# Performance work log

Hardware: AMD Instinct MI355X
Metric: run time of the kernel (lower is better)

## Reference

```python
import jax, jax.numpy as jnp
import numpy as np


def setup_inputs() -> dict:
    key = jax.random.key(0)
    k1, k2, k3, k4 = jax.random.split(key, 4)
    B, S, DIN, DOUT = 4, 4096, 512, 128
    x = jax.random.normal(k1, (B, S, DIN), dtype=jnp.float32)
    Wq = jax.random.normal(k2, (DIN, DOUT), dtype=jnp.float32) * 0.02
    Wk = jax.random.normal(k3, (DIN, DOUT), dtype=jnp.float32) * 0.02
    Wv = jax.random.normal(k4, (DIN, DOUT), dtype=jnp.float32) * 0.02
    return {"x": x, "Wq": Wq, "Wk": Wk, "Wv": Wv}


def reference(x, Wq, Wk, Wv):
    # x: [B, S, d_in]; projections (bias-free Linear)
    q = jnp.einsum('bsd,de->bse', x, Wq)  # [B, S, d_out]
    k = jnp.einsum('bsd,de->bse', x, Wk)
    v = jnp.einsum('bsd,de->bse', x, Wv)
    d_out = k.shape[-1]
    scores = jnp.einsum('bqe,bke->bqk', q, k) / jnp.sqrt(jnp.float32(d_out))  # [B, S, S]
    S = x.shape[1]
    causal = jnp.tril(jnp.ones((S, S), dtype=bool))  # True where attending allowed
    scores = jnp.where(causal[None], scores, jnp.float32(-jnp.inf))
    attn = jax.nn.softmax(scores, axis=-1)
    # dropout p=0.0 -> identity (eval mode)
    return jnp.einsum('bqk,bke->bqe', attn, v)  # [B, S, d_out]
```

## Files before the change

kernel.cpp:

```cpp
#include <hip/hip_runtime.h>

typedef __bf16 bf16x8 __attribute__((ext_vector_type(8)));
typedef float f32x4 __attribute__((ext_vector_type(4)));
typedef unsigned short u16;
typedef unsigned int u32;
typedef u16 u16x8 __attribute__((ext_vector_type(8)));
typedef u16 u16x4 __attribute__((ext_vector_type(4)));
typedef u32 u32x4 __attribute__((ext_vector_type(4)));

__device__ __forceinline__ u16 f2bf(float f) {
    u32 u = __builtin_bit_cast(u32, f);
    u += 0x7fffu + ((u >> 16) & 1u);
    return (u16)(u >> 16);
}
__device__ __forceinline__ float bf2f(u16 v) {
    return __builtin_bit_cast(float, (u32)v << 16);
}
__device__ __forceinline__ u32 cvtpk(float a, float b) {
    u32 d;
    asm("v_cvt_pk_bf16_f32 %0, %1, %2" : "=v"(d) : "v"(a), "v"(b));
    return d;
}
__device__ __forceinline__ f32x4 mfma16(u16x8 a, u16x8 b, f32x4 c) {
    return __builtin_amdgcn_mfma_f32_16x16x32_bf16(
        __builtin_bit_cast(bf16x8, a), __builtin_bit_cast(bf16x8, b), c, 0, 0, 0);
}

#define GLOAD16(SRC, DST)                                                     \
    __builtin_amdgcn_global_load_lds(                                         \
        (const __attribute__((address_space(1))) unsigned int*)(SRC),         \
        (__attribute__((address_space(3))) unsigned int*)(DST), 16, 0, 0)

__device__ __forceinline__ int ldsAddr(int r, int c) {
    return r * 128 + (((c >> 3) ^ (r & 7)) << 3) + (c & 7);
}

__global__ __launch_bounds__(256) void prep_w(
    const float* __restrict__ Wq, const float* __restrict__ Wk,
    const float* __restrict__ Wv, u16* __restrict__ wf)
{
    int flat = blockIdx.x * 256 + threadIdx.x;
    int widx = flat >> 13, rem = flat & 8191;
    int n = rem >> 10, ds = (rem >> 6) & 15, lane = rem & 63;
    int l16 = lane & 15, g = lane >> 4;
    const float* W = (widx == 0) ? Wq : (widx == 1 ? Wk : Wv);
    const float sc = (widx == 0) ? (0.08838834764831845f * 1.4426950408889634f) : 1.0f;
    u16x8 v;
    #pragma unroll
    for (int j = 0; j < 8; ++j)
        v[j] = f2bf(W[(size_t)(ds * 32 + 8 * g + j) * 128 + n * 16 + l16] * sc);
    *(u16x8*)&wf[(size_t)flat * 8] = v;
}

__global__ __launch_bounds__(256) void prep_x(
    const float* __restrict__ x, u16* __restrict__ xf)
{
    __shared__ u16 T[16 * 512];
    const int rb = blockIdx.x, t = threadIdx.x;
    const int row = t >> 4, colb = (t & 15) * 32;
    const float* src = x + (size_t)(rb * 16 + row) * 512 + colb;
    #pragma unroll
    for (int i = 0; i < 4; ++i) {
        float4 va = *(const float4*)(src + i * 8);
        float4 vb = *(const float4*)(src + i * 8 + 4);
        u16x8 v;
        v[0] = f2bf(va.x); v[1] = f2bf(va.y); v[2] = f2bf(va.z); v[3] = f2bf(va.w);
        v[4] = f2bf(vb.x); v[5] = f2bf(vb.y); v[6] = f2bf(vb.z); v[7] = f2bf(vb.w);
        int chunk = ((colb >> 3) + i) ^ (row & 7);
        *(u16x8*)&T[row * 512 + chunk * 8] = v;
    }
    __syncthreads();
    #pragma unroll
    for (int ii = 0; ii < 4; ++ii) {
        int flatF = ii * 256 + t;
        int ds = flatF >> 6, lane = flatF & 63;
        int l16 = lane & 15, g = lane >> 4;
        int chunk = (4 * ds + g) ^ (l16 & 7);
        u16x8 v = *(const u16x8*)&T[l16 * 512 + chunk * 8];
        *(u16x8*)&xf[(((size_t)rb * 16 + ds) * 64 + lane) * 8] = v;
    }
}

__global__ __launch_bounds__(256) void qkv2(
    const u16* __restrict__ xf, const u16* __restrict__ wf,
    u16* __restrict__ Qf, u16* __restrict__ Kf, u16* __restrict__ Vf)
{
    __shared__ u16 T4[4][16 * 128];
    const int tid = threadIdx.x, lane = tid & 63, wid = tid >> 6;
    const int g = lane >> 4, l16 = lane & 15;
    const int widx = blockIdx.y;
    const int rb0 = (blockIdx.x * 128 + wid * 32) >> 4;
    const u16* WfB = wf + (size_t)widx * 8192 * 8;
    u16* T = T4[wid];

    const f32x4 fz = {0.f, 0.f, 0.f, 0.f};
    f32x4 acc0[8], acc1[8];
    #pragma unroll
    for (int n = 0; n < 8; ++n) { acc0[n] = fz; acc1[n] = fz; }

    #pragma unroll 4
    for (int ds = 0; ds < 16; ++ds) {
        u16x8 a0 = *(const u16x8*)&xf[(((size_t)rb0 * 16 + ds) * 64 + lane) * 8];
        u16x8 a1 = *(const u16x8*)&xf[(((size_t)(rb0 + 1) * 16 + ds) * 64 + lane) * 8];
        #pragma unroll
        for (int n = 0; n < 8; ++n) {
            u16x8 b = *(const u16x8*)&WfB[((size_t)(n * 16 + ds) * 64 + lane) * 8];
            acc0[n] = mfma16(a0, b, acc0[n]);
            acc1[n] = mfma16(a1, b, acc1[n]);
        }
    }

    #pragma unroll
    for (int h = 0; h < 2; ++h) {
        const int rbg = rb0 + h;
        #pragma unroll
        for (int n = 0; n < 8; ++n) {
            f32x4 a = h ? acc1[n] : acc0[n];
            #pragma unroll
            for (int r = 0; r < 4; ++r)
                T[ldsAddr(4 * g + r, n * 16 + l16)] = f2bf(a[r]);
        }
        if (widx < 2) {
            u16* dst = (widx == 0) ? Qf : Kf;
            #pragma unroll
            for (int ds = 0; ds < 4; ++ds) {
                int chunk = (4 * ds + g) ^ (l16 & 7);
                u16x8 v = *(const u16x8*)&T[l16 * 128 + chunk * 8];
                *(u16x8*)&dst[(((size_t)rbg * 4 + ds) * 64 + lane) * 8] = v;
            }
        } else {
            const int kb = rbg >> 2, ksel = (rbg >> 1) & 1, g0 = (rbg & 1) * 2;
            #pragma unroll
            for (int s = 0; s < 4; ++s) {
                int flat = s * 64 + lane;
                int e = flat >> 5, gg = (flat >> 4) & 1, l16p = flat & 15;
                u16x8 v;
                #pragma unroll
                for (int j = 0; j < 8; ++j)
                    v[j] = T[ldsAddr(8 * gg + j, e * 16 + l16p)];
                *(u16x8*)&Vf[((((size_t)kb * 2 + ksel) * 8 + e) * 64
                              + (g0 + gg) * 16 + l16p) * 8] = v;
            }
        }
    }
}

__global__ __launch_bounds__(256, 2) void attn6(
    const u16* __restrict__ Qf, const u16* __restrict__ Kf,
    const u16* __restrict__ Vf, float* __restrict__ out,
    u16* __restrict__ po, float2* __restrict__ pml, int split)
{
    __shared__ u16 lds[2][16384];
    const int tid = threadIdx.x, lane = tid & 63, wid = tid >> 6;
    const int g = lane >> 4, l16 = lane & 15;

    int b, qb, c, u;
    if (split) {
        const int xcd = blockIdx.x & 7;
        b = xcd >> 1;
        int jb = 271 - ((xcd & 1) * 136 + (blockIdx.x >> 3));
        u = 0;
        while ((u + 1) * (u + 2) <= jb) ++u;
        int r = jb - u * (u + 1);
        int hi = (r >= u + 1) ? 1 : 0;
        qb = 2 * u + hi;
        c = r - hi * (u + 1);
    } else {
        b = blockIdx.x & 3;
        qb = blockIdx.x >> 2;
        c = 0; u = 0;
    }
    const int q0 = qb * 128 + wid * 32;
    const int k_lo = c * 256;
    const int k_hi = min(k_lo + (split ? 256 : 4096), qb * 128 + 128);
    const int nch = u + 1;
    const int wklen = q0 + 32;

    {
        const u16* src;
        if (wid < 2) src = Kf + (size_t)(b * 256 + (k_lo >> 4)) * 2048 + wid * 4096;
        else         src = Vf + (size_t)(b * 64 + (k_lo >> 6)) * 8192 + (wid - 2) * 4096;
        u16* dst = &lds[0][wid * 4096];
        #pragma unroll
        for (int j = 0; j < 8; ++j)
            GLOAD16(src + j * 512 + lane * 8, dst + j * 512);
    }
    const int rbq = b * 256 + qb * 8 + wid * 2;
    u16x8 qf0[4], qf1[4];
    #pragma unroll
    for (int ds = 0; ds < 4; ++ds) {
        qf0[ds] = *(const u16x8*)&Qf[(((size_t)rbq * 4 + ds) * 64 + lane) * 8];
        qf1[ds] = *(const u16x8*)&Qf[(((size_t)(rbq + 1) * 4 + ds) * 64 + lane) * 8];
    }

    const f32x4 fz = {0.f, 0.f, 0.f, 0.f};
    f32x4 o0[8], o1[8];
    #pragma unroll
    for (int e = 0; e < 8; ++e) { o0[e] = fz; o1[e] = fz; }
    float m0 = -3e38f, m1 = -3e38f, l0 = 0.f, l1 = 0.f;

    const int srcA = l16 + ((g & 1) << 5);
    const int srcB = srcA + 16;
    const bool hiSel = (g >= 2);

    __syncthreads();

    int bufsel = 0;
    for (int k0 = k_lo; k0 < k_hi; k0 += 64) {
        if (k0 + 64 < k_hi) {
            const u16* src;
            if (wid < 2) src = Kf + (size_t)(b * 256 + ((k0 + 64) >> 4)) * 2048 + wid * 4096;
            else         src = Vf + (size_t)(b * 64 + ((k0 + 64) >> 6)) * 8192 + (wid - 2) * 4096;
            u16* dst = &lds[bufsel ^ 1][wid * 4096];
            #pragma unroll
            for (int j = 0; j < 8; ++j)
                GLOAD16(src + j * 512 + lane * 8, dst + j * 512);
        }
        if (k0 < wklen) {
            const u16* Kl = &lds[bufsel][0];
            const u16* Vl = &lds[bufsel][8192];
            f32x4 st0[4], st1[4];
            #pragma unroll
            for (int kt = 0; kt < 4; ++kt) {
                st0[kt] = fz; st1[kt] = fz;
                #pragma unroll
                for (int ds = 0; ds < 4; ++ds) {
                    u16x8 kf = *(const u16x8*)&Kl[(kt * 4 + ds) * 512 + lane * 8];
                    st0[kt] = mfma16(kf, qf0[ds], st0[kt]);
                    st1[kt] = mfma16(kf, qf1[ds], st1[kt]);
                }
            }
            if (k0 + 63 > q0) {
                int qg = q0 + l16;
                #pragma unroll
                for (int kt = 0; kt < 4; ++kt)
                    #pragma unroll
                    for (int r = 0; r < 4; ++r)
                        if (k0 + kt * 16 + g * 4 + r > qg) st0[kt][r] = -1e30f;
            }
            if (k0 + 63 > q0 + 16) {
                int qg = q0 + 16 + l16;
                #pragma unroll
                for (int kt = 0; kt < 4; ++kt)
                    #pragma unroll
                    for (int r = 0; r < 4; ++r)
                        if (k0 + kt * 16 + g * 4 + r > qg) st1[kt][r] = -1e30f;
            }
            u32 pk0[4][2], pk1[4][2];
            {
                float pm = -3e38f;
                #pragma unroll
                for (int kt = 0; kt < 4; ++kt)
                    pm = fmaxf(pm, fmaxf(fmaxf(st0[kt][0], st0[kt][1]), fmaxf(st0[kt][2], st0[kt][3])));
                pm = fmaxf(pm, __shfl_xor(pm, 16));
                pm = fmaxf(pm, __shfl_xor(pm, 32));
                if (!__all(pm - m0 <= 10.0f)) {
                    float mnew = fmaxf(m0, pm);
                    float alpha = exp2f(m0 - mnew);
                    l0 *= alpha;
                    #pragma unroll
                    for (int e = 0; e < 8; ++e)
                        #pragma unroll
                        for (int r = 0; r < 4; ++r) o0[e][r] *= alpha;
                    m0 = mnew;
                }
                float lsum = 0.f;
                #pragma unroll
                for (int kt = 0; kt < 4; ++kt) {
                    float p0 = exp2f(st0[kt][0] - m0), p1 = exp2f(st0[kt][1] - m0);
                    float p2 = exp2f(st0[kt][2] - m0), p3 = exp2f(st0[kt][3] - m0);
                    lsum += (p0 + p1) + (p2 + p3);
                    pk0[kt][0] = cvtpk(p0, p1);
                    pk0[kt][1] = cvtpk(p2, p3);
                }
                lsum += __shfl_xor(lsum, 16);
                lsum += __shfl_xor(lsum, 32);
                l0 += lsum;
            }
            {
                float pm = -3e38f;
                #pragma unroll
                for (int kt = 0; kt < 4; ++kt)
                    pm = fmaxf(pm, fmaxf(fmaxf(st1[kt][0], st1[kt][1]), fmaxf(st1[kt][2], st1[kt][3])));
                pm = fmaxf(pm, __shfl_xor(pm, 16));
                pm = fmaxf(pm, __shfl_xor(pm, 32));
                if (!__all(pm - m1 <= 10.0f)) {
                    float mnew = fmaxf(m1, pm);
                    float alpha = exp2f(m1 - mnew);
                    l1 *= alpha;
                    #pragma unroll
                    for (int e = 0; e < 8; ++e)
                        #pragma unroll
                        for (int r = 0; r < 4; ++r) o1[e][r] *= alpha;
                    m1 = mnew;
                }
                float lsum = 0.f;
                #pragma unroll
                for (int kt = 0; kt < 4; ++kt) {
                    float p0 = exp2f(st1[kt][0] - m1), p1 = exp2f(st1[kt][1] - m1);
                    float p2 = exp2f(st1[kt][2] - m1), p3 = exp2f(st1[kt][3] - m1);
                    lsum += (p0 + p1) + (p2 + p3);
                    pk1[kt][0] = cvtpk(p0, p1);
                    pk1[kt][1] = cvtpk(p2, p3);
                }
                lsum += __shfl_xor(lsum, 16);
                lsum += __shfl_xor(lsum, 32);
                l1 += lsum;
            }
            #pragma unroll
            for (int ksel = 0; ksel < 2; ++ksel) {
                u32 a0 = __shfl((int)pk0[2 * ksel][0], srcA), b0 = __shfl((int)pk0[2 * ksel + 1][0], srcA);
                u32 a1 = __shfl((int)pk0[2 * ksel][1], srcA), b1 = __shfl((int)pk0[2 * ksel + 1][1], srcA);
                u32 a2 = __shfl((int)pk0[2 * ksel][0], srcB), b2 = __shfl((int)pk0[2 * ksel + 1][0], srcB);
                u32 a3 = __shfl((int)pk0[2 * ksel][1], srcB), b3 = __shfl((int)pk0[2 * ksel + 1][1], srcB);
                u32x4 d0 = { hiSel ? b0 : a0, hiSel ? b1 : a1, hiSel ? b2 : a2, hiSel ? b3 : a3 };
                u16x8 pf0 = __builtin_bit_cast(u16x8, d0);
                u32 c0 = __shfl((int)pk1[2 * ksel][0], srcA), e0 = __shfl((int)pk1[2 * ksel + 1][0], srcA);
                u32 c1 = __shfl((int)pk1[2 * ksel][1], srcA), e1 = __shfl((int)pk1[2 * ksel + 1][1], srcA);
                u32 c2 = __shfl((int)pk1[2 * ksel][0], srcB), e2 = __shfl((int)pk1[2 * ksel + 1][0], srcB);
                u32 c3 = __shfl((int)pk1[2 * ksel][1], srcB), e3 = __shfl((int)pk1[2 * ksel + 1][1], srcB);
                u32x4 d1 = { hiSel ? e0 : c0, hiSel ? e1 : c1, hiSel ? e2 : c2, hiSel ? e3 : c3 };
                u16x8 pf1 = __builtin_bit_cast(u16x8, d1);
                #pragma unroll
                for (int e = 0; e < 8; ++e) {
                    u16x8 vf = *(const u16x8*)&Vl[(ksel * 8 + e) * 512 + lane * 8];
                    o0[e] = mfma16(vf, pf0, o0[e]);
                    o1[e] = mfma16(vf, pf1, o1[e]);
                }
            }
        }
        __syncthreads();
        bufsel ^= 1;
    }

    if (nch == 1) {
        float inv0 = 1.0f / l0, inv1 = 1.0f / l1;
        float* op0 = out + ((size_t)b * 4096 + q0 + l16) * 128;
        float* op1 = out + ((size_t)b * 4096 + q0 + 16 + l16) * 128;
        #pragma unroll
        for (int e = 0; e < 8; ++e) {
            f32x4 v0 = o0[e], v1 = o1[e];
            #pragma unroll
            for (int r = 0; r < 4; ++r) { v0[r] *= inv0; v1[r] *= inv1; }
            *(f32x4*)&op0[e * 16 + g * 4] = v0;
            *(f32x4*)&op1[e * 16 + g * 4] = v1;
        }
    } else {
        const int slot = b * 272 + u * (u + 1) + (qb & 1) * (u + 1) + c;
        u16* pp0 = po + ((size_t)slot * 128 + wid * 32 + l16) * 128;
        u16* pp1 = pp0 + 16 * 128;
        #pragma unroll
        for (int e = 0; e < 8; ++e) {
            u16x4 v0, v1;
            #pragma unroll
            for (int r = 0; r < 4; ++r) { v0[r] = f2bf(o0[e][r]); v1[r] = f2bf(o1[e][r]); }
            *(u16x4*)&pp0[e * 16 + g * 4] = v0;
            *(u16x4*)&pp1[e * 16 + g * 4] = v1;
        }
        if (g == 0) {
            pml[(size_t)slot * 128 + wid * 32 + l16] = make_float2(m0, l0);
            pml[(size_t)slot * 128 + wid * 32 + 16 + l16] = make_float2(m1, l1);
        }
    }
}

__global__ __launch_bounds__(256) void merge6(
    const u16* __restrict__ po, const float2* __restrict__ pml,
    float* __restrict__ out)
{
    int gid = blockIdx.x * 256 + threadIdx.x;
    int colg = gid & 31;
    int rowid = gid >> 5;
    int b = rowid / 3840;
    int rr = rowid - b * 3840;
    int qb = (rr >> 7) + 2;
    int qr = rr & 127;
    int u = qb >> 1;
    int nch = u + 1;
    int slot0 = b * 272 + u * (u + 1) + (qb & 1) * (u + 1);

    float ms = -3e38f;
    #pragma unroll 1
    for (int cc = 0; cc < nch; ++cc)
        ms = fmaxf(ms, pml[(size_t)(slot0 + cc) * 128 + qr].x);
    float den = 0.f;
    f32x4 num = {0.f, 0.f, 0.f, 0.f};
    #pragma unroll 1
    for (int cc = 0; cc < nch; ++cc) {
        float2 ml = pml[(size_t)(slot0 + cc) * 128 + qr];
        float w = exp2f(ml.x - ms);
        den += w * ml.y;
        u16x4 pv = *(const u16x4*)&po[((size_t)(slot0 + cc) * 128 + qr) * 128 + colg * 4];
        #pragma unroll
        for (int j = 0; j < 4; ++j) num[j] += w * bf2f(pv[j]);
    }
    float inv = 1.0f / den;
    f32x4 res = { num[0] * inv, num[1] * inv, num[2] * inv, num[3] * inv };
    *(f32x4*)&out[((size_t)b * 4096 + qb * 128 + qr) * 128 + colg * 4] = res;
}

extern "C" void kernel_launch(void* const* d_in, const int* in_sizes, int n_in,
                              void* d_out, int out_size, void* d_ws, size_t ws_size,
                              hipStream_t stream) {
    (void)in_sizes; (void)n_in; (void)out_size;
    const float* x  = (const float*)d_in[0];
    const float* Wq = (const float*)d_in[1];
    const float* Wk = (const float*)d_in[2];
    const float* Wv = (const float*)d_in[3];
    float* out = (float*)d_out;

    u16* Qf = (u16*)d_ws;
    u16* Kf = Qf + 2097152;
    u16* Vf = Kf + 2097152;
    u16* xf = Vf + 2097152;
    u16* wf = xf + 8388608;
    u16* po = xf;
    float2* pml = (float2*)(po + (size_t)1088 * 128 * 128);

    const size_t fixed_b = (size_t)3 * 2097152 * 2;
    const size_t part_b  = (size_t)1088 * 128 * (128 * 2 + 8);
    const int split = (ws_size >= fixed_b + part_b) ? 1 : 0;

    prep_w<<<96, 256, 0, stream>>>(Wq, Wk, Wv, wf);
    prep_x<<<1024, 256, 0, stream>>>(x, xf);
    qkv2<<<dim3(128, 3), 256, 0, stream>>>(xf, wf, Qf, Kf, Vf);
    attn6<<<split ? 1088 : 128, 256, 0, stream>>>(Qf, Kf, Vf, out, po, pml, split);
    if (split) merge6<<<1920, 256, 0, stream>>>(po, pml, out);
}
```

Baseline: 89.96 us.

## Double attention query tile to 256 rows with 8-wave blocks

The attention kernel now uses 512-thread blocks of 8 waves covering 256 query rows, so each K/V tile staged in LDS serves twice as many queries. The split-K work decomposition is re-indexed to a triangular layout over 256-row query blocks (544 blocks instead of 1088), and the merge kernel and partial buffers are resized to match. The aim is to cut K/V global-to-LDS traffic per query and the number of partial results to merge. In exchange there are fewer blocks to fill the GPU, and the wider causal diagonal tile wastes more masked work per block.

```diff
diff --git a/kernel.cpp b/kernel.cpp
--- a/kernel.cpp
+++ b/kernel.cpp
@@ -145,7 +145,7 @@
     }
 }
 
-__global__ __launch_bounds__(256, 2) void attn6(
+__global__ __launch_bounds__(512, 4) void attn8(
     const u16* __restrict__ Qf, const u16* __restrict__ Kf,
     const u16* __restrict__ Vf, float* __restrict__ out,
     u16* __restrict__ po, float2* __restrict__ pml, int split)
@@ -154,38 +154,40 @@
     const int tid = threadIdx.x, lane = tid & 63, wid = tid >> 6;
     const int g = lane >> 4, l16 = lane & 15;
 
-    int b, qb, c, u;
+    int b, qb, c, nch, jb;
     if (split) {
         const int xcd = blockIdx.x & 7;
         b = xcd >> 1;
-        int jb = 271 - ((xcd & 1) * 136 + (blockIdx.x >> 3));
-        u = 0;
-        while ((u + 1) * (u + 2) <= jb) ++u;
-        int r = jb - u * (u + 1);
-        int hi = (r >= u + 1) ? 1 : 0;
-        qb = 2 * u + hi;
-        c = r - hi * (u + 1);
+        jb = 135 - ((xcd & 1) * 68 + (blockIdx.x >> 3));
+        qb = 0;
+        while (((qb + 1) * (qb + 2)) >> 1 <= jb) ++qb;
+        c = jb - ((qb * (qb + 1)) >> 1);
+        nch = qb + 1;
     } else {
         b = blockIdx.x & 3;
         qb = blockIdx.x >> 2;
-        c = 0; u = 0;
-    }
-    const int q0 = qb * 128 + wid * 32;
+        c = 0; nch = 1; jb = 0;
+    }
+    const int q0 = qb * 256 + wid * 32;
     const int k_lo = c * 256;
-    const int k_hi = min(k_lo + (split ? 256 : 4096), qb * 128 + 128);
-    const int nch = u + 1;
+    const int k_hi = min(k_lo + (split ? 256 : 4096), qb * 256 + 256);
     const int wklen = q0 + 32;
 
     {
         const u16* src;
-        if (wid < 2) src = Kf + (size_t)(b * 256 + (k_lo >> 4)) * 2048 + wid * 4096;
-        else         src = Vf + (size_t)(b * 64 + (k_lo >> 6)) * 8192 + (wid - 2) * 4096;
-        u16* dst = &lds[0][wid * 4096];
-        #pragma unroll
-        for (int j = 0; j < 8; ++j)
+        u16* dst;
+        if (wid < 4) {
+            src = Kf + (size_t)(b * 256 + (k_lo >> 4) + wid) * 2048;
+            dst = &lds[0][wid * 2048];
+        } else {
+            src = Vf + (size_t)(b * 64 + (k_lo >> 6)) * 8192 + (wid - 4) * 2048;
+            dst = &lds[0][8192 + (wid - 4) * 2048];
+        }
+        #pragma unroll
+        for (int j = 0; j < 4; ++j)
             GLOAD16(src + j * 512 + lane * 8, dst + j * 512);
     }
-    const int rbq = b * 256 + qb * 8 + wid * 2;
+    const int rbq = b * 256 + qb * 16 + wid * 2;
     u16x8 qf0[4], qf1[4];
     #pragma unroll
     for (int ds = 0; ds < 4; ++ds) {
@@ -209,11 +211,16 @@
     for (int k0 = k_lo; k0 < k_hi; k0 += 64) {
         if (k0 + 64 < k_hi) {
             const u16* src;
-            if (wid < 2) src = Kf + (size_t)(b * 256 + ((k0 + 64) >> 4)) * 2048 + wid * 4096;
-            else         src = Vf + (size_t)(b * 64 + ((k0 + 64) >> 6)) * 8192 + (wid - 2) * 4096;
-            u16* dst = &lds[bufsel ^ 1][wid * 4096];
-            #pragma unroll
-            for (int j = 0; j < 8; ++j)
+            u16* dst;
+            if (wid < 4) {
+                src = Kf + (size_t)(b * 256 + ((k0 + 64) >> 4) + wid) * 2048;
+                dst = &lds[bufsel ^ 1][wid * 2048];
+            } else {
+                src = Vf + (size_t)(b * 64 + ((k0 + 64) >> 6)) * 8192 + (wid - 4) * 2048;
+                dst = &lds[bufsel ^ 1][8192 + (wid - 4) * 2048];
+            }
+            #pragma unroll
+            for (int j = 0; j < 4; ++j)
                 GLOAD16(src + j * 512 + lane * 8, dst + j * 512);
         }
         if (k0 < wklen) {
@@ -346,8 +353,8 @@
             *(f32x4*)&op1[e * 16 + g * 4] = v1;
         }
     } else {
-        const int slot = b * 272 + u * (u + 1) + (qb & 1) * (u + 1) + c;
-        u16* pp0 = po + ((size_t)slot * 128 + wid * 32 + l16) * 128;
+        const int slot = b * 136 + jb;
+        u16* pp0 = po + ((size_t)slot * 256 + wid * 32 + l16) * 128;
         u16* pp1 = pp0 + 16 * 128;
         #pragma unroll
         for (int e = 0; e < 8; ++e) {
@@ -358,13 +365,13 @@
             *(u16x4*)&pp1[e * 16 + g * 4] = v1;
         }
         if (g == 0) {
-            pml[(size_t)slot * 128 + wid * 32 + l16] = make_float2(m0, l0);
-            pml[(size_t)slot * 128 + wid * 32 + 16 + l16] = make_float2(m1, l1);
-        }
-    }
-}
-
-__global__ __launch_bounds__(256) void merge6(
+            pml[(size_t)slot * 256 + wid * 32 + l16] = make_float2(m0, l0);
+            pml[(size_t)slot * 256 + wid * 32 + 16 + l16] = make_float2(m1, l1);
+        }
+    }
+}
+
+__global__ __launch_bounds__(256) void merge8(
     const u16* __restrict__ po, const float2* __restrict__ pml,
     float* __restrict__ out)
 {
@@ -373,30 +380,29 @@
     int rowid = gid >> 5;
     int b = rowid / 3840;
     int rr = rowid - b * 3840;
-    int qb = (rr >> 7) + 2;
-    int qr = rr & 127;
-    int u = qb >> 1;
-    int nch = u + 1;
-    int slot0 = b * 272 + u * (u + 1) + (qb & 1) * (u + 1);
+    int qb = (rr >> 8) + 1;
+    int qr = rr & 255;
+    int nch = qb + 1;
+    int slot0 = b * 136 + ((qb * (qb + 1)) >> 1);
 
     float ms = -3e38f;
     #pragma unroll 1
     for (int cc = 0; cc < nch; ++cc)
-        ms = fmaxf(ms, pml[(size_t)(slot0 + cc) * 128 + qr].x);
+        ms = fmaxf(ms, pml[(size_t)(slot0 + cc) * 256 + qr].x);
     float den = 0.f;
     f32x4 num = {0.f, 0.f, 0.f, 0.f};
     #pragma unroll 1
     for (int cc = 0; cc < nch; ++cc) {
-        float2 ml = pml[(size_t)(slot0 + cc) * 128 + qr];
+        float2 ml = pml[(size_t)(slot0 + cc) * 256 + qr];
         float w = exp2f(ml.x - ms);
         den += w * ml.y;
-        u16x4 pv = *(const u16x4*)&po[((size_t)(slot0 + cc) * 128 + qr) * 128 + colg * 4];
+        u16x4 pv = *(const u16x4*)&po[((size_t)(slot0 + cc) * 256 + qr) * 128 + colg * 4];
         #pragma unroll
         for (int j = 0; j < 4; ++j) num[j] += w * bf2f(pv[j]);
     }
     float inv = 1.0f / den;
     f32x4 res = { num[0] * inv, num[1] * inv, num[2] * inv, num[3] * inv };
-    *(f32x4*)&out[((size_t)b * 4096 + qb * 128 + qr) * 128 + colg * 4] = res;
+    *(f32x4*)&out[((size_t)b * 4096 + qb * 256 + qr) * 128 + colg * 4] = res;
 }
 
 extern "C" void kernel_launch(void* const* d_in, const int* in_sizes, int n_in,
@@ -415,15 +421,15 @@
     u16* xf = Vf + 2097152;
     u16* wf = xf + 8388608;
     u16* po = xf;
-    float2* pml = (float2*)(po + (size_t)1088 * 128 * 128);
+    float2* pml = (float2*)(po + (size_t)544 * 256 * 128);
 
     const size_t fixed_b = (size_t)3 * 2097152 * 2;
-    const size_t part_b  = (size_t)1088 * 128 * (128 * 2 + 8);
+    const size_t part_b  = (size_t)544 * 256 * (128 * 2 + 8);
     const int split = (ws_size >= fixed_b + part_b) ? 1 : 0;
 
     prep_w<<<96, 256, 0, stream>>>(Wq, Wk, Wv, wf);
     prep_x<<<1024, 256, 0, stream>>>(x, xf);
     qkv2<<<dim3(128, 3), 256, 0, stream>>>(xf, wf, Qf, Kf, Vf);
-    attn6<<<split ? 1088 : 128, 256, 0, stream>>>(Qf, Kf, Vf, out, po, pml, split);
-    if (split) merge6<<<1920, 256, 0, stream>>>(po, pml, out);
-}
+    attn8<<<split ? 544 : 64, 512, 0, stream>>>(Qf, Kf, Vf, out, po, pml, split);
+    if (split) merge8<<<1920, 256, 0, stream>>>(po, pml, out);
+}
```

Result: slower. 150.3 us (+67.1%).
